# Kernel tuning notes

Hardware: AMD Instinct MI355X
Metric: run time of the kernel (lower is better)

The kernel has to match this reference:

```python
import jax, jax.numpy as jnp
import numpy as np

COST_CLASS, COST_OBJECTNESS, COST_GIOU, COST_CENTER = 1.0, 0.5, 2.0, 1.0
B, Q, G, C = 32, 4096, 32, 128


def setup_inputs() -> dict:
    key = jax.random.key(0)
    ks = jax.random.split(key, 6)
    return {
        "sem_cls_prob": jax.random.uniform(ks[0], (B, Q, C), jnp.float32),
        "objectness_prob": jax.random.uniform(ks[1], (B, Q), jnp.float32),
        "center_dist": jax.random.uniform(ks[2], (B, Q, G), jnp.float32),
        "gious": jax.random.uniform(ks[3], (B, Q, G), jnp.float32) * 2.0 - 1.0,  # gIoU in [-1,1]
        "gt_box_sem_cls_label": jax.random.randint(ks[4], (B, G), 0, C).astype(jnp.int64),
        "nactual_gt": jax.random.randint(ks[5], (B,), 1, G + 1).astype(jnp.int64),
    }


def _lsa(Cmat):
    """Jonker-Volgenant shortest augmenting path Hungarian.
    Cmat: [n, m] float64 with n <= m. Returns p: [m+1] int64, p[j] = row matched
    to column j (or -1), index m is the virtual start column. Equivalent to
    scipy.optimize.linear_sum_assignment on Cmat (modulo ties)."""
    n, m = Cmat.shape
    u = np.zeros(n, np.float64)
    v = np.zeros(m + 1, np.float64)
    p = np.full(m + 1, -1, np.int64)
    way = np.zeros(m, np.int64)
    for i in range(n):
        p[m] = i
        j0 = m
        minv = np.full(m, np.inf)
        used = np.zeros(m + 1, bool)
        while True:
            used[j0] = True
            i0 = p[j0]
            cur = Cmat[i0] - u[i0] - v[:m]            # vectorized Dijkstra relaxation
            better = (~used[:m]) & (cur < minv)
            minv = np.where(better, cur, minv)
            way = np.where(better, j0, way)
            mv = np.where(used[:m], np.inf, minv)
            j1 = int(np.argmin(mv))
            delta = mv[j1]
            rows = p[used]                            # matched rows of used cols (distinct)
            u[rows] += delta
            v[used] -= delta
            minv = np.where(used[:m], minv, minv - delta)
            j0 = j1
            if p[j0] == -1:
                break
        while j0 != m:                                # augment along the path
            j1 = way[j0]
            p[j0] = p[j1]
            j0 = j1
    return p


def hungarian_assign(final_cost, nactual_gt):
    """final_cost: np [B,Q,G]; emulates the per-batch scipy loop of the module."""
    Bn, Qn, _ = final_cost.shape
    per_prop = np.zeros((Bn, Qn), np.int64)
    mask = np.zeros((Bn, Qn), np.float32)
    for b in range(Bn):
        ng = int(nactual_gt[b])
        if ng > 0:
            p = _lsa(final_cost[b, :, :ng].T.astype(np.float64))  # [ng, Q]
            cols = np.nonzero(p[:Qn] >= 0)[0]
            per_prop[b, cols] = p[cols]
            mask[b, cols] = 1.0
    return per_prop, mask


def build_cost(sem_cls_prob, objectness_prob, center_dist, gious, gt_box_sem_cls_label):
    Bn, Qn, _ = sem_cls_prob.shape
    Gn = gt_box_sem_cls_label.shape[1]
    idx = jnp.broadcast_to(gt_box_sem_cls_label[:, None, :], (Bn, Qn, Gn))
    class_mat = -jnp.take_along_axis(sem_cls_prob, idx, axis=2)        # [B,Q,G]
    return (COST_CLASS * class_mat
            - COST_OBJECTNESS * objectness_prob[:, :, None]
            + COST_CENTER * center_dist
            - COST_GIOU * gious)


def reference(sem_cls_prob, objectness_prob, center_dist, gious, gt_box_sem_cls_label, nactual_gt):
    final_cost = build_cost(sem_cls_prob, objectness_prob, center_dist, gious, gt_box_sem_cls_label)
    cost_np = np.asarray(jax.device_get(final_cost))
    per_prop, mask = hungarian_assign(cost_np, np.asarray(jax.device_get(nactual_gt)))
    return jnp.asarray(per_prop), jnp.asarray(mask)
```

## Files before the change

### kernel.cpp

```cpp
#include <hip/hip_runtime.h>
#include <math.h>

#define NB   32
#define BQ   4096
#define GMAX 32
#define NC   128
#define BS   512
#define CPT  (BQ / BS)
#define NWAVE (BS / 64)

#define TQ   32
#define BBS  256
#define NTILE (BQ / TQ)

#define COST_BYTES ((size_t)NB * GMAX * BQ * 4)

__launch_bounds__(BBS)
__global__ void build_cost_kernel(const float* __restrict__ sem,
                                  const float* __restrict__ objp,
                                  const float* __restrict__ cent,
                                  const float* __restrict__ giou,
                                  const int*   __restrict__ labels,
                                  const int*   __restrict__ nact,
                                  float* __restrict__ cost,
                                  unsigned long long* __restrict__ pmin)
{
    const int b  = blockIdx.y;
    const int qt = blockIdx.x;
    const int q0 = qt * TQ;
    const int tid = threadIdx.x;

    __shared__ float sem_sh[TQ][NC + 1];
    __shared__ float cent_sh[TQ][GMAX + 1];
    __shared__ float giou_sh[TQ][GMAX + 1];
    __shared__ int lab_sh[GMAX];

    if (tid < GMAX) lab_sh[tid] = labels[b * GMAX + tid];
    const int ng = nact[b];

    const float4* semb = (const float4*)(sem + ((size_t)b * BQ + q0) * NC);
#pragma unroll
    for (int r = tid; r < TQ * NC / 4; r += BBS) {
        float4 vv = semb[r];
        int e = r * 4;
        int qq = e >> 7;
        int cc = e & (NC - 1);
        sem_sh[qq][cc]     = vv.x;
        sem_sh[qq][cc + 1] = vv.y;
        sem_sh[qq][cc + 2] = vv.z;
        sem_sh[qq][cc + 3] = vv.w;
    }
    {
        const float4* centb = (const float4*)(cent + ((size_t)b * BQ + q0) * GMAX);
        const float4* gioub = (const float4*)(giou + ((size_t)b * BQ + q0) * GMAX);
        int r = tid;
        float4 cv = centb[r];
        float4 gv = gioub[r];
        int e = r * 4;
        int qq = e >> 5;
        int ii = e & (GMAX - 1);
        cent_sh[qq][ii]     = cv.x;
        cent_sh[qq][ii + 1] = cv.y;
        cent_sh[qq][ii + 2] = cv.z;
        cent_sh[qq][ii + 3] = cv.w;
        giou_sh[qq][ii]     = gv.x;
        giou_sh[qq][ii + 1] = gv.y;
        giou_sh[qq][ii + 2] = gv.z;
        giou_sh[qq][ii + 3] = gv.w;
    }
    __syncthreads();

    const int qi = tid & (TQ - 1);
    const int ig = tid >> 5;
    const int q  = q0 + qi;
    const float ho = __fmul_rn(0.5f, objp[b * BQ + q]);

    for (int i = ig; i < ng; i += 8) {
        float pcls = sem_sh[qi][lab_sh[i]];
        float ce   = cent_sh[qi][i];
        float gi   = giou_sh[qi][i];
        float c = __fsub_rn(__fadd_rn(__fsub_rn(-pcls, ho), ce),
                            __fmul_rn(2.0f, gi));
        cost[((size_t)b * GMAX + i) * BQ + q] = c;

        unsigned cbits = __float_as_uint(c);
        unsigned mono  = (cbits & 0x80000000u) ? ~cbits : (cbits | 0x80000000u);
        unsigned long long key = ((unsigned long long)mono << 32) | (unsigned)q;
#pragma unroll
        for (int off = 16; off >= 1; off >>= 1) {
            unsigned long long ok = __shfl_down(key, off, 32);
            if (ok < key) key = ok;
        }
        if (qi == 0) pmin[((size_t)b * GMAX + i) * NTILE + qt] = key;
    }
}

__launch_bounds__(BS, 1)
__global__ void matcher_kernel(const float* __restrict__ cost,
                               const unsigned long long* __restrict__ pmin,
                               const int*   __restrict__ nact,
                               float* __restrict__ out)
{
    const int b    = blockIdx.x;
    const int tid  = threadIdx.x;
    const int m    = BQ;
    const int wave = tid >> 6;
    const int lane = tid & 63;

    __shared__ __align__(16) short p_lds[BQ + 8];
    __shared__ __align__(16) unsigned short way_lds[BQ];
    __shared__ double u_lds[GMAX];
    __shared__ double   redv[2][NWAVE];
    __shared__ unsigned redpk[2][NWAVE];
    __shared__ int    step_i0[GMAX + 2];
    __shared__ double step_D[GMAX + 2];
    __shared__ float  rmin_v[GMAX];
    __shared__ int    rmin_j[GMAX];
    __shared__ int    unmatched[GMAX];
    __shared__ int    s_nunm;

    for (int k = tid; k < BQ + 8; k += BS) p_lds[k] = -1;
    const int ng = nact[b];
    const float* cb = cost + (size_t)b * GMAX * BQ;
    __syncthreads();

    {
        const unsigned long long* pb = pmin + (size_t)b * GMAX * NTILE;
        for (int r = wave; r < ng; r += NWAVE) {
            const unsigned long long* row = pb + (size_t)r * NTILE;
            unsigned long long k0 = row[lane];
            unsigned long long k1 = row[lane + 64];
            unsigned long long key = (k1 < k0) ? k1 : k0;
#pragma unroll
            for (int off = 32; off >= 1; off >>= 1) {
                unsigned long long ok = __shfl_down(key, off, 64);
                if (ok < key) key = ok;
            }
            if (lane == 0) {
                unsigned mono = (unsigned)(key >> 32);
                unsigned bits = (mono & 0x80000000u) ? (mono ^ 0x80000000u) : ~mono;
                rmin_v[r] = __uint_as_float(bits);
                rmin_j[r] = (int)(key & 0xFFFFFFFFu);
            }
        }
    }
    __syncthreads();

    if (tid < ng) u_lds[tid] = (double)rmin_v[tid];
    if (tid == 0) {
        int nu = 0;
        for (int i = 0; i < ng; i++) {
            int j = rmin_j[i];
            if (p_lds[j] < 0) p_lds[j] = (short)i;
            else unmatched[nu++] = i;
        }
        s_nunm = nu;
    }
    __syncthreads();
    const int nunm = s_nunm;

    const double INF = (double)INFINITY;
    const int jbase = tid * CPT;
    const float4* cb4 = (const float4*)cb;

    double v_reg[CPT], minv[CPT], enterD[CPT];
    int way_reg[CPT], p_reg[CPT];
#pragma unroll
    for (int k = 0; k < CPT; k++) { v_reg[k] = 0.0; way_reg[k] = m; enterD[k] = 0.0; }

    for (int t = 0; t < nunm; t++) {
        const int ri = unmatched[t];

        int4 pv = ((const int4*)p_lds)[tid];
        p_reg[0] = (int)(short)(pv.x & 0xFFFF); p_reg[1] = pv.x >> 16;
        p_reg[2] = (int)(short)(pv.y & 0xFFFF); p_reg[3] = pv.y >> 16;
        p_reg[4] = (int)(short)(pv.z & 0xFFFF); p_reg[5] = pv.z >> 16;
        p_reg[6] = (int)(short)(pv.w & 0xFFFF); p_reg[7] = pv.w >> 16;

        const float4* r4 = cb4 + (size_t)ri * (BQ / 4) + tid * 2;
        float4 c0 = r4[0];
        float4 c1 = r4[1];
        double ui0 = u_lds[ri];

#pragma unroll
        for (int k = 0; k < CPT; k++) minv[k] = INF;
        unsigned used_mask = 0;
        int i0 = ri, j0 = m, ns = 0, buf = 0, jfin;
        double D = 0.0;

        while (true) {
            float cf[CPT] = {c0.x, c0.y, c0.z, c0.w, c1.x, c1.y, c1.z, c1.w};

            double bestv = INF;
            unsigned bestpk = ((unsigned)m << 8);
#pragma unroll
            for (int k = 0; k < CPT; k++) {
                bool un = !((used_mask >> k) & 1u);
                double cur = ((double)cf[k] - ui0) - v_reg[k];
                bool better = un && (cur < minv[k]);
                if (better) { minv[k] = cur; way_reg[k] = j0; }
                double mv = un ? minv[k] : INF;
                if (mv < bestv) {
                    bestv = mv;
                    bestpk = (((unsigned)(jbase + k)) << 8) | (unsigned)(p_reg[k] + 1);
                }
            }

#pragma unroll
            for (int off = 32; off >= 1; off >>= 1) {
                double   ov  = __shfl_down(bestv, off, 64);
                unsigned opk = __shfl_down(bestpk, off, 64);
                if (ov < bestv || (ov == bestv && opk < bestpk)) { bestv = ov; bestpk = opk; }
            }
            if (lane == 0) { redv[buf][wave] = bestv; redpk[buf][wave] = bestpk; }
            __syncthreads();

            double delta = redv[buf][0]; unsigned pk = redpk[buf][0];
#pragma unroll
            for (int w = 1; w < NWAVE; w++) {
                double ov = redv[buf][w]; unsigned opk = redpk[buf][w];
                if (ov < delta || (ov == delta && opk < pk)) { delta = ov; pk = opk; }
            }
            const int j1 = (int)(pk >> 8);
            const int pi = (int)(pk & 0xFFu) - 1;

            if (tid == 0) { step_i0[ns] = i0; step_D[ns] = D; }
            D += delta;
            ns++;

            if (pi < 0) { jfin = j1; break; }

            const float4* n4 = cb4 + (size_t)pi * (BQ / 4) + tid * 2;
            c0 = n4[0];
            c1 = n4[1];
            ui0 = u_lds[pi];

#pragma unroll
            for (int k = 0; k < CPT; k++)
                if (!((used_mask >> k) & 1u)) minv[k] -= delta;

            unsigned kk = (unsigned)(j1 - jbase);
            if (kk < CPT) { used_mask |= (1u << kk); enterD[kk] = D; }

            i0 = pi; j0 = j1; buf ^= 1;
        }

#pragma unroll
        for (int k = 0; k < CPT; k++)
            if ((used_mask >> k) & 1u) { v_reg[k] -= (D - enterD[k]); }

        int4 wv;
        wv.x = (way_reg[0] & 0xFFFF) | (way_reg[1] << 16);
        wv.y = (way_reg[2] & 0xFFFF) | (way_reg[3] << 16);
        wv.z = (way_reg[4] & 0xFFFF) | (way_reg[5] << 16);
        wv.w = (way_reg[6] & 0xFFFF) | (way_reg[7] << 16);
        ((int4*)way_lds)[tid] = wv;

        __syncthreads();
        if (tid < ns) u_lds[step_i0[tid]] += D - step_D[tid];
        if (tid == 0) {
            int jc = jfin;
            while (jc != m) {
                int jp = (int)way_lds[jc];
                p_lds[jc] = (jp == m) ? (short)ri : p_lds[jp];
                jc = jp;
            }
        }
        __syncthreads();
    }

#pragma unroll
    for (int k = 0; k < CPT; k++) {
        int j = jbase + k;
        short pj = p_lds[j];
        out[(size_t)b * BQ + j] = (pj >= 0) ? (float)pj : 0.0f;
        out[(size_t)NB * BQ + (size_t)b * BQ + j] = (pj >= 0) ? 1.0f : 0.0f;
    }
}

extern "C" void kernel_launch(void* const* d_in, const int* in_sizes, int n_in,
                              void* d_out, int out_size, void* d_ws, size_t ws_size,
                              hipStream_t stream) {
    const float* sem    = (const float*)d_in[0];
    const float* objp   = (const float*)d_in[1];
    const float* cent   = (const float*)d_in[2];
    const float* giou   = (const float*)d_in[3];
    const int*   labels = (const int*)d_in[4];
    const int*   nact   = (const int*)d_in[5];
    float* out  = (float*)d_out;
    float* cost = (float*)d_ws;
    unsigned long long* pmin =
        (unsigned long long*)((char*)d_ws + COST_BYTES);

    dim3 bgrid(NTILE, NB);
    build_cost_kernel<<<bgrid, BBS, 0, stream>>>(sem, objp, cent, giou,
                                                 labels, nact, cost, pmin);
    matcher_kernel<<<NB, BS, 0, stream>>>(cost, pmin, nact, out);
}
```

Baseline: 139.8 us.

## Fuse cost build and matcher via last-block-per-batch atomic counter

Merges the cost-building kernel and the Hungarian matcher into one launch. Each tile block bumps a per-batch global counter, and the last block to finish for a batch runs the assignment. This removes the second kernel launch and the gap between the two kernels, and lets matching for early batches overlap cost building for other batches. In exchange, the matcher now runs on 256 threads with 16 columns per thread instead of 512 with 8, which lengthens each per-step serial scan and raises register pressure, and the counter is never reset and relies on modulo arithmetic across calls.

```diff
diff --git a/kernel.cpp b/kernel.cpp
--- a/kernel.cpp
+++ b/kernel.cpp
@@ -5,38 +5,63 @@
 #define BQ   4096
 #define GMAX 32
 #define NC   128
-#define BS   512
-#define CPT  (BQ / BS)
-#define NWAVE (BS / 64)
-
+#define BBS  256
 #define TQ   32
-#define BBS  256
 #define NTILE (BQ / TQ)
+#define CPT  (BQ / BBS)
+#define NWAVE (BBS / 64)
 
 #define COST_BYTES ((size_t)NB * GMAX * BQ * 4)
 
-__launch_bounds__(BBS)
-__global__ void build_cost_kernel(const float* __restrict__ sem,
-                                  const float* __restrict__ objp,
-                                  const float* __restrict__ cent,
-                                  const float* __restrict__ giou,
-                                  const int*   __restrict__ labels,
-                                  const int*   __restrict__ nact,
-                                  float* __restrict__ cost,
-                                  unsigned long long* __restrict__ pmin)
+__device__ int g_cnt[NB];
+
+struct BuildSmem {
+    float sem_sh[TQ][NC + 1];
+    float cent_sh[TQ][GMAX + 1];
+    float giou_sh[TQ][GMAX + 1];
+    int   lab_sh[GMAX];
+};
+struct MatchSmem {
+    short p[BQ + 8];
+    unsigned short way[BQ];
+    double u[GMAX];
+    double redv[2][NWAVE];
+    double step_D[GMAX + 2];
+    unsigned redpk[2][NWAVE];
+    int    step_i0[GMAX + 2];
+    float  rmin_v[GMAX];
+    int    rmin_j[GMAX];
+    int    unmatched[GMAX];
+    int    nunm;
+};
+union Smem {
+    BuildSmem b;
+    MatchSmem m;
+};
+
+__launch_bounds__(BBS, 4)
+__global__ void fused_kernel(const float* __restrict__ sem,
+                             const float* __restrict__ objp,
+                             const float* __restrict__ cent,
+                             const float* __restrict__ giou,
+                             const int*   __restrict__ labels,
+                             const int*   __restrict__ nact,
+                             float* __restrict__ cost,
+                             unsigned long long* __restrict__ pmin,
+                             float* __restrict__ out)
 {
-    const int b  = blockIdx.y;
-    const int qt = blockIdx.x;
-    const int q0 = qt * TQ;
+    __shared__ Smem S;
+    __shared__ int s_last;
+
+    const int b   = blockIdx.y;
+    const int qt  = blockIdx.x;
+    const int q0  = qt * TQ;
     const int tid = threadIdx.x;
-
-    __shared__ float sem_sh[TQ][NC + 1];
-    __shared__ float cent_sh[TQ][GMAX + 1];
-    __shared__ float giou_sh[TQ][GMAX + 1];
-    __shared__ int lab_sh[GMAX];
-
-    if (tid < GMAX) lab_sh[tid] = labels[b * GMAX + tid];
-    const int ng = nact[b];
+    const int wave = tid >> 6;
+    const int lane = tid & 63;
+    const int ng  = nact[b];
+
+    if (tid < GMAX) S.b.lab_sh[tid] = labels[b * GMAX + tid];
 
     const float4* semb = (const float4*)(sem + ((size_t)b * BQ + q0) * NC);
 #pragma unroll
@@ -45,10 +70,10 @@
         int e = r * 4;
         int qq = e >> 7;
         int cc = e & (NC - 1);
-        sem_sh[qq][cc]     = vv.x;
-        sem_sh[qq][cc + 1] = vv.y;
-        sem_sh[qq][cc + 2] = vv.z;
-        sem_sh[qq][cc + 3] = vv.w;
+        S.b.sem_sh[qq][cc]     = vv.x;
+        S.b.sem_sh[qq][cc + 1] = vv.y;
+        S.b.sem_sh[qq][cc + 2] = vv.z;
+        S.b.sem_sh[qq][cc + 3] = vv.w;
     }
     {
         const float4* centb = (const float4*)(cent + ((size_t)b * BQ + q0) * GMAX);
@@ -59,70 +84,58 @@
         int e = r * 4;
         int qq = e >> 5;
         int ii = e & (GMAX - 1);
-        cent_sh[qq][ii]     = cv.x;
-        cent_sh[qq][ii + 1] = cv.y;
-        cent_sh[qq][ii + 2] = cv.z;
-        cent_sh[qq][ii + 3] = cv.w;
-        giou_sh[qq][ii]     = gv.x;
-        giou_sh[qq][ii + 1] = gv.y;
-        giou_sh[qq][ii + 2] = gv.z;
-        giou_sh[qq][ii + 3] = gv.w;
-    }
-    __syncthreads();
-
-    const int qi = tid & (TQ - 1);
-    const int ig = tid >> 5;
-    const int q  = q0 + qi;
-    const float ho = __fmul_rn(0.5f, objp[b * BQ + q]);
-
-    for (int i = ig; i < ng; i += 8) {
-        float pcls = sem_sh[qi][lab_sh[i]];
-        float ce   = cent_sh[qi][i];
-        float gi   = giou_sh[qi][i];
-        float c = __fsub_rn(__fadd_rn(__fsub_rn(-pcls, ho), ce),
-                            __fmul_rn(2.0f, gi));
-        cost[((size_t)b * GMAX + i) * BQ + q] = c;
-
-        unsigned cbits = __float_as_uint(c);
-        unsigned mono  = (cbits & 0x80000000u) ? ~cbits : (cbits | 0x80000000u);
-        unsigned long long key = ((unsigned long long)mono << 32) | (unsigned)q;
-#pragma unroll
-        for (int off = 16; off >= 1; off >>= 1) {
-            unsigned long long ok = __shfl_down(key, off, 32);
-            if (ok < key) key = ok;
+        S.b.cent_sh[qq][ii]     = cv.x;
+        S.b.cent_sh[qq][ii + 1] = cv.y;
+        S.b.cent_sh[qq][ii + 2] = cv.z;
+        S.b.cent_sh[qq][ii + 3] = cv.w;
+        S.b.giou_sh[qq][ii]     = gv.x;
+        S.b.giou_sh[qq][ii + 1] = gv.y;
+        S.b.giou_sh[qq][ii + 2] = gv.z;
+        S.b.giou_sh[qq][ii + 3] = gv.w;
+    }
+    __syncthreads();
+
+    {
+        const int qi = tid & (TQ - 1);
+        const int ig = tid >> 5;
+        const int q  = q0 + qi;
+        const float ho = __fmul_rn(0.5f, objp[b * BQ + q]);
+
+        for (int i = ig; i < ng; i += 8) {
+            float pcls = S.b.sem_sh[qi][S.b.lab_sh[i]];
+            float ce   = S.b.cent_sh[qi][i];
+            float gi   = S.b.giou_sh[qi][i];
+            float c = __fsub_rn(__fadd_rn(__fsub_rn(-pcls, ho), ce),
+                                __fmul_rn(2.0f, gi));
+            cost[((size_t)b * GMAX + i) * BQ + q] = c;
+
+            unsigned cbits = __float_as_uint(c);
+            unsigned mono  = (cbits & 0x80000000u) ? ~cbits : (cbits | 0x80000000u);
+            unsigned long long key = ((unsigned long long)mono << 32) | (unsigned)q;
+#pragma unroll
+            for (int off = 16; off >= 1; off >>= 1) {
+                unsigned long long ok = __shfl_down(key, off, 32);
+                if (ok < key) key = ok;
+            }
+            if (qi == 0) pmin[((size_t)b * GMAX + i) * NTILE + qt] = key;
         }
-        if (qi == 0) pmin[((size_t)b * GMAX + i) * NTILE + qt] = key;
-    }
-}
-
-__launch_bounds__(BS, 1)
-__global__ void matcher_kernel(const float* __restrict__ cost,
-                               const unsigned long long* __restrict__ pmin,
-                               const int*   __restrict__ nact,
-                               float* __restrict__ out)
-{
-    const int b    = blockIdx.x;
-    const int tid  = threadIdx.x;
-    const int m    = BQ;
-    const int wave = tid >> 6;
-    const int lane = tid & 63;
-
-    __shared__ __align__(16) short p_lds[BQ + 8];
-    __shared__ __align__(16) unsigned short way_lds[BQ];
-    __shared__ double u_lds[GMAX];
-    __shared__ double   redv[2][NWAVE];
-    __shared__ unsigned redpk[2][NWAVE];
-    __shared__ int    step_i0[GMAX + 2];
-    __shared__ double step_D[GMAX + 2];
-    __shared__ float  rmin_v[GMAX];
-    __shared__ int    rmin_j[GMAX];
-    __shared__ int    unmatched[GMAX];
-    __shared__ int    s_nunm;
-
-    for (int k = tid; k < BQ + 8; k += BS) p_lds[k] = -1;
-    const int ng = nact[b];
+    }
+
+    __syncthreads();
+    if (tid == 0) {
+        __threadfence();
+        int old = __hip_atomic_fetch_add(&g_cnt[b], 1, __ATOMIC_ACQ_REL,
+                                         __HIP_MEMORY_SCOPE_AGENT);
+        s_last = ((old & (NTILE - 1)) == (NTILE - 1)) ? 1 : 0;
+    }
+    __syncthreads();
+    if (!s_last) return;
+    __threadfence();
+
+    const int m = BQ;
     const float* cb = cost + (size_t)b * GMAX * BQ;
-    __syncthreads();
+
+    for (int k = tid; k < BQ + 8; k += BBS) S.m.p[k] = -1;
 
     {
         const unsigned long long* pb = pmin + (size_t)b * GMAX * NTILE;
@@ -139,140 +152,158 @@
             if (lane == 0) {
                 unsigned mono = (unsigned)(key >> 32);
                 unsigned bits = (mono & 0x80000000u) ? (mono ^ 0x80000000u) : ~mono;
-                rmin_v[r] = __uint_as_float(bits);
-                rmin_j[r] = (int)(key & 0xFFFFFFFFu);
+                S.m.rmin_v[r] = __uint_as_float(bits);
+                S.m.rmin_j[r] = (int)(key & 0xFFFFFFFFu);
             }
         }
     }
     __syncthreads();
 
-    if (tid < ng) u_lds[tid] = (double)rmin_v[tid];
+    if (tid < ng) S.m.u[tid] = (double)S.m.rmin_v[tid];
     if (tid == 0) {
         int nu = 0;
         for (int i = 0; i < ng; i++) {
-            int j = rmin_j[i];
-            if (p_lds[j] < 0) p_lds[j] = (short)i;
-            else unmatched[nu++] = i;
+            int j = S.m.rmin_j[i];
+            if (S.m.p[j] < 0) S.m.p[j] = (short)i;
+            else S.m.unmatched[nu++] = i;
         }
-        s_nunm = nu;
-    }
-    __syncthreads();
-    const int nunm = s_nunm;
-
-    const double INF = (double)INFINITY;
+        S.m.nunm = nu;
+    }
+    __syncthreads();
+    const int nunm = S.m.nunm;
+
+    if (nunm > 0) {
+        const double INF = (double)INFINITY;
+        const int jbase = tid * CPT;
+        const float4* cb4 = (const float4*)cb;
+
+        double v_reg[CPT], minv[CPT], enterD[CPT];
+        int way_reg[CPT], p_reg[CPT];
+#pragma unroll
+        for (int k = 0; k < CPT; k++) { v_reg[k] = 0.0; way_reg[k] = m; enterD[k] = 0.0; }
+
+        for (int t = 0; t < nunm; t++) {
+            const int ri = S.m.unmatched[t];
+
+            int4 pv0 = ((const int4*)S.m.p)[2 * tid];
+            int4 pv1 = ((const int4*)S.m.p)[2 * tid + 1];
+            p_reg[0]  = (int)(short)(pv0.x & 0xFFFF); p_reg[1]  = pv0.x >> 16;
+            p_reg[2]  = (int)(short)(pv0.y & 0xFFFF); p_reg[3]  = pv0.y >> 16;
+            p_reg[4]  = (int)(short)(pv0.z & 0xFFFF); p_reg[5]  = pv0.z >> 16;
+            p_reg[6]  = (int)(short)(pv0.w & 0xFFFF); p_reg[7]  = pv0.w >> 16;
+            p_reg[8]  = (int)(short)(pv1.x & 0xFFFF); p_reg[9]  = pv1.x >> 16;
+            p_reg[10] = (int)(short)(pv1.y & 0xFFFF); p_reg[11] = pv1.y >> 16;
+            p_reg[12] = (int)(short)(pv1.z & 0xFFFF); p_reg[13] = pv1.z >> 16;
+            p_reg[14] = (int)(short)(pv1.w & 0xFFFF); p_reg[15] = pv1.w >> 16;
+
+            const float4* r4 = cb4 + (size_t)ri * (BQ / 4) + tid * 4;
+            float4 c0 = r4[0];
+            float4 c1 = r4[1];
+            float4 c2 = r4[2];
+            float4 c3 = r4[3];
+            double ui0 = S.m.u[ri];
+
+#pragma unroll
+            for (int k = 0; k < CPT; k++) minv[k] = INF;
+            unsigned used_mask = 0;
+            int i0 = ri, j0 = m, ns = 0, buf = 0, jfin;
+            double D = 0.0;
+
+            while (true) {
+                float cf[CPT] = {c0.x, c0.y, c0.z, c0.w, c1.x, c1.y, c1.z, c1.w,
+                                 c2.x, c2.y, c2.z, c2.w, c3.x, c3.y, c3.z, c3.w};
+
+                double bestv = INF;
+                unsigned bestpk = ((unsigned)m << 8);
+#pragma unroll
+                for (int k = 0; k < CPT; k++) {
+                    bool un = !((used_mask >> k) & 1u);
+                    double cur = ((double)cf[k] - ui0) - v_reg[k];
+                    bool better = un && (cur < minv[k]);
+                    if (better) { minv[k] = cur; way_reg[k] = j0; }
+                    double mv = un ? minv[k] : INF;
+                    if (mv < bestv) {
+                        bestv = mv;
+                        bestpk = (((unsigned)(jbase + k)) << 8) | (unsigned)(p_reg[k] + 1);
+                    }
+                }
+
+#pragma unroll
+                for (int off = 32; off >= 1; off >>= 1) {
+                    double   ov  = __shfl_down(bestv, off, 64);
+                    unsigned opk = __shfl_down(bestpk, off, 64);
+                    if (ov < bestv || (ov == bestv && opk < bestpk)) { bestv = ov; bestpk = opk; }
+                }
+                if (lane == 0) { S.m.redv[buf][wave] = bestv; S.m.redpk[buf][wave] = bestpk; }
+                __syncthreads();
+
+                double delta = S.m.redv[buf][0]; unsigned pk = S.m.redpk[buf][0];
+#pragma unroll
+                for (int w = 1; w < NWAVE; w++) {
+                    double ov = S.m.redv[buf][w]; unsigned opk = S.m.redpk[buf][w];
+                    if (ov < delta || (ov == delta && opk < pk)) { delta = ov; pk = opk; }
+                }
+                const int j1 = (int)(pk >> 8);
+                const int pi = (int)(pk & 0xFFu) - 1;
+
+                if (tid == 0) { S.m.step_i0[ns] = i0; S.m.step_D[ns] = D; }
+                D += delta;
+                ns++;
+
+                if (pi < 0) { jfin = j1; break; }
+
+                const float4* n4 = cb4 + (size_t)pi * (BQ / 4) + tid * 4;
+                c0 = n4[0];
+                c1 = n4[1];
+                c2 = n4[2];
+                c3 = n4[3];
+                ui0 = S.m.u[pi];
+
+#pragma unroll
+                for (int k = 0; k < CPT; k++)
+                    if (!((used_mask >> k) & 1u)) minv[k] -= delta;
+
+                unsigned kk = (unsigned)(j1 - jbase);
+                if (kk < CPT) { used_mask |= (1u << kk); enterD[kk] = D; }
+
+                i0 = pi; j0 = j1; buf ^= 1;
+            }
+
+#pragma unroll
+            for (int k = 0; k < CPT; k++)
+                if ((used_mask >> k) & 1u) { v_reg[k] -= (D - enterD[k]); }
+
+            int4 w0, w1;
+            w0.x = (way_reg[0]  & 0xFFFF) | (way_reg[1]  << 16);
+            w0.y = (way_reg[2]  & 0xFFFF) | (way_reg[3]  << 16);
+            w0.z = (way_reg[4]  & 0xFFFF) | (way_reg[5]  << 16);
+            w0.w = (way_reg[6]  & 0xFFFF) | (way_reg[7]  << 16);
+            w1.x = (way_reg[8]  & 0xFFFF) | (way_reg[9]  << 16);
+            w1.y = (way_reg[10] & 0xFFFF) | (way_reg[11] << 16);
+            w1.z = (way_reg[12] & 0xFFFF) | (way_reg[13] << 16);
+            w1.w = (way_reg[14] & 0xFFFF) | (way_reg[15] << 16);
+            ((int4*)S.m.way)[2 * tid]     = w0;
+            ((int4*)S.m.way)[2 * tid + 1] = w1;
+
+            __syncthreads();
+            if (tid < ns) S.m.u[S.m.step_i0[tid]] += D - S.m.step_D[tid];
+            if (tid == 0) {
+                int jc = jfin;
+                while (jc != m) {
+                    int jp = (int)S.m.way[jc];
+                    S.m.p[jc] = (jp == m) ? (short)ri : S.m.p[jp];
+                    jc = jp;
+                }
+            }
+            __syncthreads();
+        }
+    }
+
     const int jbase = tid * CPT;
-    const float4* cb4 = (const float4*)cb;
-
-    double v_reg[CPT], minv[CPT], enterD[CPT];
-    int way_reg[CPT], p_reg[CPT];
-#pragma unroll
-    for (int k = 0; k < CPT; k++) { v_reg[k] = 0.0; way_reg[k] = m; enterD[k] = 0.0; }
-
-    for (int t = 0; t < nunm; t++) {
-        const int ri = unmatched[t];
-
-        int4 pv = ((const int4*)p_lds)[tid];
-        p_reg[0] = (int)(short)(pv.x & 0xFFFF); p_reg[1] = pv.x >> 16;
-        p_reg[2] = (int)(short)(pv.y & 0xFFFF); p_reg[3] = pv.y >> 16;
-        p_reg[4] = (int)(short)(pv.z & 0xFFFF); p_reg[5] = pv.z >> 16;
-        p_reg[6] = (int)(short)(pv.w & 0xFFFF); p_reg[7] = pv.w >> 16;
-
-        const float4* r4 = cb4 + (size_t)ri * (BQ / 4) + tid * 2;
-        float4 c0 = r4[0];
-        float4 c1 = r4[1];
-        double ui0 = u_lds[ri];
-
-#pragma unroll
-        for (int k = 0; k < CPT; k++) minv[k] = INF;
-        unsigned used_mask = 0;
-        int i0 = ri, j0 = m, ns = 0, buf = 0, jfin;
-        double D = 0.0;
-
-        while (true) {
-            float cf[CPT] = {c0.x, c0.y, c0.z, c0.w, c1.x, c1.y, c1.z, c1.w};
-
-            double bestv = INF;
-            unsigned bestpk = ((unsigned)m << 8);
-#pragma unroll
-            for (int k = 0; k < CPT; k++) {
-                bool un = !((used_mask >> k) & 1u);
-                double cur = ((double)cf[k] - ui0) - v_reg[k];
-                bool better = un && (cur < minv[k]);
-                if (better) { minv[k] = cur; way_reg[k] = j0; }
-                double mv = un ? minv[k] : INF;
-                if (mv < bestv) {
-                    bestv = mv;
-                    bestpk = (((unsigned)(jbase + k)) << 8) | (unsigned)(p_reg[k] + 1);
-                }
-            }
-
-#pragma unroll
-            for (int off = 32; off >= 1; off >>= 1) {
-                double   ov  = __shfl_down(bestv, off, 64);
-                unsigned opk = __shfl_down(bestpk, off, 64);
-                if (ov < bestv || (ov == bestv && opk < bestpk)) { bestv = ov; bestpk = opk; }
-            }
-            if (lane == 0) { redv[buf][wave] = bestv; redpk[buf][wave] = bestpk; }
-            __syncthreads();
-
-            double delta = redv[buf][0]; unsigned pk = redpk[buf][0];
-#pragma unroll
-            for (int w = 1; w < NWAVE; w++) {
-                double ov = redv[buf][w]; unsigned opk = redpk[buf][w];
-                if (ov < delta || (ov == delta && opk < pk)) { delta = ov; pk = opk; }
-            }
-            const int j1 = (int)(pk >> 8);
-            const int pi = (int)(pk & 0xFFu) - 1;
-
-            if (tid == 0) { step_i0[ns] = i0; step_D[ns] = D; }
-            D += delta;
-            ns++;
-
-            if (pi < 0) { jfin = j1; break; }
-
-            const float4* n4 = cb4 + (size_t)pi * (BQ / 4) + tid * 2;
-            c0 = n4[0];
-            c1 = n4[1];
-            ui0 = u_lds[pi];
-
-#pragma unroll
-            for (int k = 0; k < CPT; k++)
-                if (!((used_mask >> k) & 1u)) minv[k] -= delta;
-
-            unsigned kk = (unsigned)(j1 - jbase);
-            if (kk < CPT) { used_mask |= (1u << kk); enterD[kk] = D; }
-
-            i0 = pi; j0 = j1; buf ^= 1;
-        }
-
-#pragma unroll
-        for (int k = 0; k < CPT; k++)
-            if ((used_mask >> k) & 1u) { v_reg[k] -= (D - enterD[k]); }
-
-        int4 wv;
-        wv.x = (way_reg[0] & 0xFFFF) | (way_reg[1] << 16);
-        wv.y = (way_reg[2] & 0xFFFF) | (way_reg[3] << 16);
-        wv.z = (way_reg[4] & 0xFFFF) | (way_reg[5] << 16);
-        wv.w = (way_reg[6] & 0xFFFF) | (way_reg[7] << 16);
-        ((int4*)way_lds)[tid] = wv;
-
-        __syncthreads();
-        if (tid < ns) u_lds[step_i0[tid]] += D - step_D[tid];
-        if (tid == 0) {
-            int jc = jfin;
-            while (jc != m) {
-                int jp = (int)way_lds[jc];
-                p_lds[jc] = (jp == m) ? (short)ri : p_lds[jp];
-                jc = jp;
-            }
-        }
-        __syncthreads();
-    }
-
 #pragma unroll
     for (int k = 0; k < CPT; k++) {
         int j = jbase + k;
-        short pj = p_lds[j];
+        short pj = S.m.p[j];
         out[(size_t)b * BQ + j] = (pj >= 0) ? (float)pj : 0.0f;
         out[(size_t)NB * BQ + (size_t)b * BQ + j] = (pj >= 0) ? 1.0f : 0.0f;
     }
@@ -292,8 +323,7 @@
     unsigned long long* pmin =
         (unsigned long long*)((char*)d_ws + COST_BYTES);
 
-    dim3 bgrid(NTILE, NB);
-    build_cost_kernel<<<bgrid, BBS, 0, stream>>>(sem, objp, cent, giou,
-                                                 labels, nact, cost, pmin);
-    matcher_kernel<<<NB, BS, 0, stream>>>(cost, pmin, nact, out);
+    dim3 grid(NTILE, NB);
+    fused_kernel<<<grid, BBS, 0, stream>>>(sem, objp, cent, giou,
+                                           labels, nact, cost, pmin, out);
 }
```

Result: slower. 537.2 us (+284.2%).

## Gather class probabilities directly instead of staging full sem tile in LDS

Applied to the files above, without the earlier changes.

The cost-build kernel no longer copies the whole 32x128 semantic-probability tile into shared memory. Each thread instead gathers only the labelled class entries it needs straight from global memory, with up to four loads issued ahead of the compute loop. This is meant to cut the dominant read traffic of the full sem tensor down to roughly ng scattered reads per query. The cost stores become nontemporal, and the matcher's p_lds initialisation uses vectorised int4 stores. The gathers are uncoalesced, strided by 512 bytes across lanes, which may waste cache-line bandwidth.

```diff
diff --git a/kernel.cpp b/kernel.cpp
--- a/kernel.cpp
+++ b/kernel.cpp
@@ -30,7 +30,6 @@
     const int q0 = qt * TQ;
     const int tid = threadIdx.x;
 
-    __shared__ float sem_sh[TQ][NC + 1];
     __shared__ float cent_sh[TQ][GMAX + 1];
     __shared__ float giou_sh[TQ][GMAX + 1];
     __shared__ int lab_sh[GMAX];
@@ -38,18 +37,6 @@
     if (tid < GMAX) lab_sh[tid] = labels[b * GMAX + tid];
     const int ng = nact[b];
 
-    const float4* semb = (const float4*)(sem + ((size_t)b * BQ + q0) * NC);
-#pragma unroll
-    for (int r = tid; r < TQ * NC / 4; r += BBS) {
-        float4 vv = semb[r];
-        int e = r * 4;
-        int qq = e >> 7;
-        int cc = e & (NC - 1);
-        sem_sh[qq][cc]     = vv.x;
-        sem_sh[qq][cc + 1] = vv.y;
-        sem_sh[qq][cc + 2] = vv.z;
-        sem_sh[qq][cc + 3] = vv.w;
-    }
     {
         const float4* centb = (const float4*)(cent + ((size_t)b * BQ + q0) * GMAX);
         const float4* gioub = (const float4*)(giou + ((size_t)b * BQ + q0) * GMAX);
@@ -74,14 +61,24 @@
     const int ig = tid >> 5;
     const int q  = q0 + qi;
     const float ho = __fmul_rn(0.5f, objp[b * BQ + q]);
-
-    for (int i = ig; i < ng; i += 8) {
-        float pcls = sem_sh[qi][lab_sh[i]];
-        float ce   = cent_sh[qi][i];
-        float gi   = giou_sh[qi][i];
-        float c = __fsub_rn(__fadd_rn(__fsub_rn(-pcls, ho), ce),
+    const float* semrow = sem + ((size_t)b * BQ + q) * NC;
+
+    float pc[4];
+#pragma unroll
+    for (int k = 0; k < 4; k++) {
+        int i = ig + 8 * k;
+        if (i < ng) pc[k] = semrow[lab_sh[i]];
+    }
+
+#pragma unroll
+    for (int k = 0; k < 4; k++) {
+        int i = ig + 8 * k;
+        if (i >= ng) break;
+        float ce = cent_sh[qi][i];
+        float gi = giou_sh[qi][i];
+        float c = __fsub_rn(__fadd_rn(__fsub_rn(-pc[k], ho), ce),
                             __fmul_rn(2.0f, gi));
-        cost[((size_t)b * GMAX + i) * BQ + q] = c;
+        __builtin_nontemporal_store(c, &cost[((size_t)b * GMAX + i) * BQ + q]);
 
         unsigned cbits = __float_as_uint(c);
         unsigned mono  = (cbits & 0x80000000u) ? ~cbits : (cbits | 0x80000000u);
@@ -119,7 +116,11 @@
     __shared__ int    unmatched[GMAX];
     __shared__ int    s_nunm;
 
-    for (int k = tid; k < BQ + 8; k += BS) p_lds[k] = -1;
+    {
+        int4 mone; mone.x = mone.y = mone.z = mone.w = -1;
+        ((int4*)p_lds)[tid] = mone;
+        if (tid < 4) ((int*)(p_lds + BQ))[tid] = -1;
+    }
     const int ng = nact[b];
     const float* cb = cost + (size_t)b * GMAX * BQ;
     __syncthreads();
```

Result: no change. 138.8 us (median of 2 runs) (-0.8%).
